# Performance work log

Hardware: AMD Instinct MI355X
Metric: run time of the kernel (lower is better)

Reference implementation:

```python
import jax, jax.numpy as jnp
import numpy as np

N_NODES = 160_000
N_EDGES = 640_000
N_GRAPHS = 8_000
IN_FEATS = 74
HID = 63
MAX_DEG = 10
PRED_HID = 128
PRED_DIM = 256
BN_EPS = 1e-5
N_LAYERS = 3
PARAM_NAMES = ['W0', 'b0', 'gamma0', 'beta0', 'W1', 'b1', 'gamma1', 'beta1', 'W2', 'b2', 'gamma2', 'beta2', 'W_ng', 'b_ng', 'W_tr', 'b_tr']


def setup_inputs() -> dict:
    key = jax.random.key(0)
    ks = jax.random.split(key, 20)
    inp = {}
    inp['feats'] = jax.random.normal(ks[0], (N_NODES, IN_FEATS), dtype=jnp.float32)
    inp['src'] = jax.random.randint(ks[1], (N_EDGES,), 0, N_NODES, dtype=jnp.int32)
    inp['dst'] = jax.random.randint(ks[2], (N_EDGES,), 0, N_NODES, dtype=jnp.int32)
    # sorted graph membership: 20 nodes per graph (batched molecular graphs)
    inp['graph_ids'] = jnp.repeat(jnp.arange(N_GRAPHS, dtype=jnp.int32), N_NODES // N_GRAPHS)
    dims = [IN_FEATS, HID, HID, HID]
    for l in range(N_LAYERS):
        fi, fo = dims[l], dims[l + 1]
        inp[f'W{l}'] = jax.random.normal(ks[3 + l], (MAX_DEG, fi, fo), dtype=jnp.float32) / np.float32(np.sqrt(fi))
        inp[f'b{l}'] = jnp.zeros((MAX_DEG, fo), dtype=jnp.float32)
        inp[f'gamma{l}'] = jnp.ones((fo,), dtype=jnp.float32)
        inp[f'beta{l}'] = jnp.zeros((fo,), dtype=jnp.float32)
    inp['W_ng'] = jax.random.normal(ks[10], (HID, PRED_HID), dtype=jnp.float32) / np.float32(np.sqrt(HID))
    inp['b_ng'] = jnp.zeros((PRED_HID,), dtype=jnp.float32)
    inp['W_tr'] = jax.random.normal(ks[11], (2 * PRED_HID, PRED_DIM), dtype=jnp.float32) / np.float32(np.sqrt(2 * PRED_HID))
    inp['b_tr'] = jnp.zeros((PRED_DIM,), dtype=jnp.float32)
    return inp


def _nf_layer(h, src, dst, deg_idx, W, b, gamma, beta):
    # message passing: sum of neighbor features via copy_u / fn.sum
    neigh = jax.ops.segment_sum(h[src], dst, num_segments=N_NODES)
    tot = h + neigh  # self + neighbor sum (Duvenaud neural fingerprint)
    # degree-bucketed linear: compute all MAX_DEG transforms, select per node by degree
    z_all = jnp.einsum('ni,kio->nko', tot, W) + b  # [N, MAX_DEG, out]
    z = jnp.take_along_axis(z_all, deg_idx[:, None, None], axis=1)[:, 0, :]  # [N, out]
    z = jax.nn.relu(z)
    # batchnorm over nodes (training-mode batch statistics, eps=1e-5)
    mu = jnp.mean(z, axis=0)
    var = jnp.var(z, axis=0)
    return (z - mu) * jax.lax.rsqrt(var + BN_EPS) * gamma + beta


def _forward(feats, src, dst, graph_ids, params):
    # in-degree per node, clamped to [1, MAX_DEG] -> weight bucket index
    deg = jax.ops.segment_sum(jnp.ones((N_EDGES,), jnp.float32), dst, num_segments=N_NODES)
    deg_idx = jnp.clip(deg.astype(jnp.int32), 1, MAX_DEG) - 1
    h = feats
    for l in range(N_LAYERS):
        h = _nf_layer(h, src, dst, deg_idx, params[f'W{l}'], params[f'b{l}'],
                      params[f'gamma{l}'], params[f'beta{l}'])
    # node_to_graph linear
    h = h @ params['W_ng'] + params['b_ng']  # [N, PRED_HID]
    # SumAndMax readout over each graph
    g_sum = jax.ops.segment_sum(h, graph_ids, num_segments=N_GRAPHS)
    g_max = jax.ops.segment_max(h, graph_ids, num_segments=N_GRAPHS)
    g = jnp.tanh(jnp.concatenate([g_sum, g_max], axis=-1))  # [G, 2*PRED_HID]
    return g @ params['W_tr'] + params['b_tr']  # [G, PRED_DIM]


def reference(feats, src, dst, graph_ids, W0, b0, gamma0, beta0, W1, b1, gamma1, beta1, W2, b2, gamma2, beta2, W_ng, b_ng, W_tr, b_tr):
    params = dict(zip(PARAM_NAMES, (W0, b0, gamma0, beta0, W1, b1, gamma1, beta1, W2, b2, gamma2, beta2, W_ng, b_ng, W_tr, b_tr)))
    return _forward(feats, src, dst, graph_ids, params)
```

## Files before the change

### kernel.cpp

```cpp
#include <hip/hip_runtime.h>
#include <stdint.h>
#include <math.h>

static constexpr int NN = 160000;
static constexpr int NE = 640000;
static constexpr int NG = 8000;
static constexpr int FH  = 63;
static constexpr int ZST = 64;
static constexpr int FST = 80;
static constexpr int NB  = 128;
static constexpr int LGRID = 1536;

static constexpr size_t OFF_DEGCNT = 0;
static constexpr size_t OFF_CURSOR = 640000;
static constexpr size_t OFF_BCNT   = 1280000;
static constexpr size_t OFF_SPART  = 1280064;
static constexpr size_t ZERO_BYTES = 1673280;
static constexpr size_t OFF_ROWPTR = 1673280;
static constexpr size_t OFF_BLKSUM = 2313472;
static constexpr size_t OFF_COL    = 2315520;
static constexpr size_t OFF_BLIST  = 4875520;
static constexpr size_t OFF_AFC    = 17675520;
static constexpr size_t OFF_WNG2   = 17677056;
static constexpr size_t OFF_BNG2   = 17709312;
static constexpr size_t OFF_PBLK   = 17709824;
static constexpr size_t OFF_FB     = 17710080;
static constexpr size_t OFF_Z0     = 43310080;
static constexpr size_t OFF_Z1     = 63790080;

__device__ __forceinline__ float blo(unsigned u) {
    union { unsigned i; float f; } v; v.i = u << 16; return v.f;
}
__device__ __forceinline__ float bhi(unsigned u) {
    union { unsigned i; float f; } v; v.i = u & 0xffff0000u; return v.f;
}
__device__ __forceinline__ unsigned short f2b(float f) {
    union { float f; unsigned i; } v; v.f = f;
    unsigned r = v.i + 0x7fffu + ((v.i >> 16) & 1u);
    return (unsigned short)(r >> 16);
}
__device__ __forceinline__ void acc8(float* a, uint4 q) {
    a[0] += blo(q.x); a[1] += bhi(q.x);
    a[2] += blo(q.y); a[3] += bhi(q.y);
    a[4] += blo(q.z); a[5] += bhi(q.z);
    a[6] += blo(q.w); a[7] += bhi(q.w);
}

__global__ void k_degree(const int* __restrict__ dst, int* __restrict__ degcnt) {
    int e = blockIdx.x * 256 + threadIdx.x;
    if (e < NE) atomicAdd(&degcnt[dst[e]], 1);
}

__global__ void k_scan1(const int* __restrict__ degcnt, int* __restrict__ row_ptr,
                        int* __restrict__ blksum) {
    __shared__ int s[1024];
    int t = threadIdx.x;
    int i = blockIdx.x * 1024 + t;
    int v = (i < NN) ? degcnt[i] : 0;
    s[t] = v; __syncthreads();
    for (int off = 1; off < 1024; off <<= 1) {
        int x = (t >= off) ? s[t - off] : 0;
        __syncthreads();
        s[t] += x;
        __syncthreads();
    }
    if (i < NN) row_ptr[i + 1] = s[t];
    if (t == 1023) blksum[blockIdx.x] = s[t];
}

__global__ void k_scan2(int* __restrict__ blksum, int nblk) {
    __shared__ int s[256];
    int t = threadIdx.x;
    int v = (t < nblk) ? blksum[t] : 0;
    s[t] = v; __syncthreads();
    for (int off = 1; off < 256; off <<= 1) {
        int x = (t >= off) ? s[t - off] : 0;
        __syncthreads();
        s[t] += x;
        __syncthreads();
    }
    if (t < nblk) blksum[t] = s[t] - v;
}

__global__ void k_scan3(int* __restrict__ row_ptr, const int* __restrict__ blksum) {
    int t = threadIdx.x;
    int i = blockIdx.x * 1024 + t;
    if (i < NN) row_ptr[i + 1] += blksum[blockIdx.x];
    if (i == 0) row_ptr[0] = 0;
}

__global__ void k_cast(const float* __restrict__ feats, unsigned short* __restrict__ fb) {
    int i = blockIdx.x * 256 + threadIdx.x;
    if (i >= NN * FST) return;
    int n = i / FST, c = i - n * FST;
    float v = (c < 74) ? feats[n * 74 + c] : 0.f;
    union { float f; unsigned u; } x; x.f = v;
    unsigned r = x.u + 0x7fffu + ((x.u >> 16) & 1u);
    fb[i] = (unsigned short)(r >> 16);
}

__global__ void __launch_bounds__(1024) k_bucket(
        const int* __restrict__ degcnt, const int* __restrict__ row_ptr,
        int* __restrict__ bcnt, int2* __restrict__ blist) {
    __shared__ int scnt[10], sbase[10];
    int tid = threadIdx.x;
    if (tid < 10) scnt[tid] = 0;
    __syncthreads();
    int n = blockIdx.x * 1024 + tid;
    int k = 0, pos = 0;
    bool v = (n < NN);
    int rp = 0;
    if (v) {
        int d = degcnt[n];
        rp = row_ptr[n];
        k = (d < 1) ? 0 : ((d > 10) ? 9 : d - 1);
        pos = atomicAdd(&scnt[k], 1);
    }
    __syncthreads();
    if (tid < 10) sbase[tid] = scnt[tid] ? atomicAdd(&bcnt[tid], scnt[tid]) : 0;
    __syncthreads();
    if (v) blist[k * NN + sbase[k] + pos] = make_int2(n, rp);
}

__global__ void k_prep(const int* __restrict__ bcnt, int* __restrict__ pblk) {
    if (threadIdx.x == 0) {
        int s = 0; pblk[0] = 0;
        for (int k = 0; k < 10; ++k) { s += (bcnt[k] + NB - 1) / NB; pblk[k + 1] = s; }
    }
}

__global__ void k_fill(const int* __restrict__ src, const int* __restrict__ dst,
                       const int* __restrict__ row_ptr, int* __restrict__ cursor,
                       int* __restrict__ col) {
    int e = blockIdx.x * 256 + threadIdx.x;
    if (e >= NE) return;
    int d = dst[e];
    int pos = row_ptr[d] + atomicAdd(&cursor[d], 1);
    col[pos] = src[e];
}

template<int FI, int IST, bool AFF>
__global__ void __launch_bounds__(256, 2) k_layer(
    const unsigned short* __restrict__ in,
    const float* __restrict__ aff,
    const int* __restrict__ row_ptr, const int* __restrict__ col,
    const int* __restrict__ bcnt, const int2* __restrict__ blist,
    const int* __restrict__ pblk,
    const float* __restrict__ W, const float* __restrict__ B,
    unsigned short* __restrict__ zout, float* __restrict__ spart)
{
    constexpr int CH = IST / 8;
    __shared__ float sW[FI * 63 + 64];
    __shared__ float sTot[4][80][8];
    __shared__ int   sN[4][8];
    __shared__ float sRed[2][4][64];

    int b = blockIdx.x;
    if (b >= pblk[10]) return;
    int k = 0;
#pragma unroll
    for (int i = 1; i <= 9; ++i) k += (b >= pblk[i]) ? 1 : 0;
    int base = (b - pblk[k]) * NB;
    int cnt = bcnt[k];
    if (base >= cnt) return;

    int tid = threadIdx.x;
    int wave = tid >> 6, lane = tid & 63;
    int t = lane >> 3, r = lane & 7;

    const float* Wk = W + (size_t)k * FI * 63;
#pragma unroll 4
    for (int i = tid; i < FI * 63; i += 256) sW[i] = Wk[i];
    __syncthreads();

    const uint4* inq = (const uint4*)in;
    float bterm = (lane < 63) ? B[k * 63 + lane] : 0.f;
    float lsum = 0.f, lsq = 0.f;

#pragma unroll 1
    for (int it = 0; it < NB / 32; ++it) {
        int idx = base + it * 32 + wave * 8 + t;
        if (base + it * 32 >= cnt) break;
        bool val = (idx < cnt);
        int2 bl = blist[k * NN + (val ? idx : (cnt - 1))];
        int n = bl.x, rs = bl.y;
        int dg = (k >= 1 && k <= 8) ? (k + 1) : (row_ptr[n + 1] - rs);
        if (r == 0) sN[wave][t] = val ? n : -1;

        float a[8] = {0.f, 0.f, 0.f, 0.f, 0.f, 0.f, 0.f, 0.f};
        {
            uint4 q = inq[(size_t)n * CH + r];
            acc8(a, q);
        }
        int d = 0;
#pragma unroll 1
        for (; d + 4 <= dg; d += 4) {
            int c0 = col[rs + d], c1 = col[rs + d + 1];
            int c2 = col[rs + d + 2], c3 = col[rs + d + 3];
            uint4 q0 = inq[(size_t)c0 * CH + r];
            uint4 q1 = inq[(size_t)c1 * CH + r];
            uint4 q2 = inq[(size_t)c2 * CH + r];
            uint4 q3 = inq[(size_t)c3 * CH + r];
            acc8(a, q0); acc8(a, q1); acc8(a, q2); acc8(a, q3);
        }
#pragma unroll 1
        for (; d < dg; ++d) {
            int c = col[rs + d];
            uint4 q = inq[(size_t)c * CH + r];
            acc8(a, q);
        }

        if constexpr (IST == 80) {
            float e2[8] = {0.f, 0.f, 0.f, 0.f, 0.f, 0.f, 0.f, 0.f};
            if (r < 2) {
                uint4 q = inq[(size_t)n * CH + 8 + r];
                acc8(e2, q);
                int d2 = 0;
#pragma unroll 1
                for (; d2 < dg; ++d2) {
                    int c = col[rs + d2];
                    uint4 p = inq[(size_t)c * CH + 8 + r];
                    acc8(e2, p);
                }
#pragma unroll
                for (int j = 0; j < 8; ++j) sTot[wave][64 + 8 * r + j][t] = e2[j];
            }
        }

        if constexpr (AFF) {
            const float4* af = (const float4*)aff;
            float4 A0 = af[2 * r], A1 = af[2 * r + 1];
            float4 C0 = af[16 + 2 * r], C1 = af[16 + 2 * r + 1];
            float dp1 = (float)(dg + 1);
            a[0] = A0.x * a[0] + dp1 * C0.x;  a[1] = A0.y * a[1] + dp1 * C0.y;
            a[2] = A0.z * a[2] + dp1 * C0.z;  a[3] = A0.w * a[3] + dp1 * C0.w;
            a[4] = A1.x * a[4] + dp1 * C1.x;  a[5] = A1.y * a[5] + dp1 * C1.y;
            a[6] = A1.z * a[6] + dp1 * C1.z;  a[7] = A1.w * a[7] + dp1 * C1.w;
        }

#pragma unroll
        for (int j = 0; j < 8; ++j) sTot[wave][8 * r + j][t] = a[j];

        float acc[8];
#pragma unroll
        for (int i = 0; i < 8; ++i) acc[i] = bterm;
#pragma unroll 4
        for (int j = 0; j < FI; ++j) {
            float w = sW[j * 63 + lane];
            float4 u = *(const float4*)&sTot[wave][j][0];
            float4 v = *(const float4*)&sTot[wave][j][4];
            acc[0] = fmaf(u.x, w, acc[0]); acc[1] = fmaf(u.y, w, acc[1]);
            acc[2] = fmaf(u.z, w, acc[2]); acc[3] = fmaf(u.w, w, acc[3]);
            acc[4] = fmaf(v.x, w, acc[4]); acc[5] = fmaf(v.y, w, acc[5]);
            acc[6] = fmaf(v.z, w, acc[6]); acc[7] = fmaf(v.w, w, acc[7]);
        }

#pragma unroll
        for (int tt = 0; tt < 8; ++tt) {
            int nn = sN[wave][tt];
            float z = fmaxf(acc[tt], 0.f);
            if (nn >= 0 && lane < 63) {
                zout[(size_t)nn * ZST + lane] = f2b(z);
                lsum += z; lsq += z * z;
            }
        }
    }

    sRed[0][wave][lane] = lsum;
    sRed[1][wave][lane] = lsq;
    __syncthreads();
    if (wave == 0 && lane < 63) {
        float s = sRed[0][0][lane] + sRed[0][1][lane] + sRed[0][2][lane] + sRed[0][3][lane];
        float q = sRed[1][0][lane] + sRed[1][1][lane] + sRed[1][2][lane] + sRed[1][3][lane];
        float* sp = spart + (size_t)(blockIdx.x & 255) * 128;
        atomicAdd(&sp[lane], s);
        atomicAdd(&sp[64 + lane], q);
    }
}

__global__ void k_bn(const float* __restrict__ spart, const float* __restrict__ gamma,
                     const float* __restrict__ beta, float* __restrict__ afc) {
    int o = threadIdx.x;
    if (o >= 63) return;
    double s = 0.0, q = 0.0;
    for (int cp = 0; cp < 256; ++cp) {
        s += (double)spart[cp * 128 + o];
        q += (double)spart[cp * 128 + 64 + o];
    }
    double mu  = s / NN;
    double var = q / NN - mu * mu;
    float a = (float)((double)gamma[o] / sqrt(var + 1e-5));
    float c = (float)((double)beta[o] - mu * (double)a);
    afc[o] = a;
    afc[64 + o] = c;
}

__global__ void k_fold(const float* __restrict__ W_ng, const float* __restrict__ b_ng,
                       const float* __restrict__ afc2, float* __restrict__ Wng2,
                       float* __restrict__ bng2) {
    int o = threadIdx.x;
    float acc = b_ng[o];
    for (int j = 0; j < 63; ++j) {
        float w = W_ng[j * 128 + o];
        Wng2[j * 128 + o] = afc2[j] * w;
        acc = fmaf(afc2[64 + j], w, acc);
    }
    bng2[o] = acc;
}

__global__ void __launch_bounds__(256) k_graph(
    const unsigned short* __restrict__ Z2, const float* __restrict__ Wng2,
    const float* __restrict__ bng2, const float* __restrict__ W_tr,
    const float* __restrict__ b_tr, float* __restrict__ out)
{
    __shared__ float sWng[64 * 128];
    __shared__ unsigned short sZ[4 * 20 * 64];
    __shared__ float sT[4][256];
    int tid = threadIdx.x;
    int g0 = blockIdx.x * 4;

#pragma unroll 4
    for (int i = tid; i < 64 * 128; i += 256)
        sWng[i] = (i < 63 * 128) ? Wng2[i] : 0.f;
    {
        const uint4* zsrc = (const uint4*)(Z2 + (size_t)g0 * 20 * ZST);
        uint4* zdst = (uint4*)sZ;
#pragma unroll 3
        for (int i = tid; i < 640; i += 256) zdst[i] = zsrc[i];
    }
    if (tid < 80) sZ[tid * 64 + 63] = 0;
    __syncthreads();

    int wv = tid >> 6, lane = tid & 63;
    const unsigned short* zg = sZ + wv * 1280;

    float acc0[20], acc1[20];
    float b0v = bng2[lane], b1v = bng2[lane + 64];
#pragma unroll
    for (int i = 0; i < 20; ++i) { acc0[i] = b0v; acc1[i] = b1v; }
#pragma unroll 1
    for (int jb = 0; jb < 16; ++jb) {
        int j = jb * 4;
        float w00 = sWng[(j + 0) * 128 + lane], w01 = sWng[(j + 0) * 128 + 64 + lane];
        float w10 = sWng[(j + 1) * 128 + lane], w11 = sWng[(j + 1) * 128 + 64 + lane];
        float w20 = sWng[(j + 2) * 128 + lane], w21 = sWng[(j + 2) * 128 + 64 + lane];
        float w30 = sWng[(j + 3) * 128 + lane], w31 = sWng[(j + 3) * 128 + 64 + lane];
#pragma unroll
        for (int i = 0; i < 20; ++i) {
            uint2 zz = *(const uint2*)&zg[i * 64 + j];
            float z0 = blo(zz.x), z1 = bhi(zz.x);
            float z2 = blo(zz.y), z3 = bhi(zz.y);
            acc0[i] = fmaf(z0, w00, acc0[i]); acc1[i] = fmaf(z0, w01, acc1[i]);
            acc0[i] = fmaf(z1, w10, acc0[i]); acc1[i] = fmaf(z1, w11, acc1[i]);
            acc0[i] = fmaf(z2, w20, acc0[i]); acc1[i] = fmaf(z2, w21, acc1[i]);
            acc0[i] = fmaf(z3, w30, acc0[i]); acc1[i] = fmaf(z3, w31, acc1[i]);
        }
    }
    float s0 = 0.f, s1 = 0.f, m0 = -1e30f, m1 = -1e30f;
#pragma unroll
    for (int i = 0; i < 20; ++i) {
        s0 += acc0[i]; s1 += acc1[i];
        m0 = fmaxf(m0, acc0[i]); m1 = fmaxf(m1, acc1[i]);
    }
    sT[wv][lane]       = tanhf(s0);
    sT[wv][lane + 64]  = tanhf(s1);
    sT[wv][128 + lane] = tanhf(m0);
    sT[wv][192 + lane] = tanhf(m1);
    __syncthreads();

    int d = tid;
    float acc[4];
    float bt = b_tr[d];
#pragma unroll
    for (int gl = 0; gl < 4; ++gl) acc[gl] = bt;
#pragma unroll 16
    for (int q = 0; q < 256; ++q) {
        float w = W_tr[q * 256 + d];
#pragma unroll
        for (int gl = 0; gl < 4; ++gl) acc[gl] = fmaf(sT[gl][q], w, acc[gl]);
    }
#pragma unroll
    for (int gl = 0; gl < 4; ++gl) out[(size_t)(g0 + gl) * 256 + d] = acc[gl];
}

extern "C" void kernel_launch(void* const* d_in, const int* in_sizes, int n_in,
                              void* d_out, int out_size, void* d_ws, size_t ws_size,
                              hipStream_t stream) {
    const float* feats = (const float*)d_in[0];
    const int*   src   = (const int*)d_in[1];
    const int*   dst   = (const int*)d_in[2];
    const float* W0 = (const float*)d_in[4];
    const float* b0 = (const float*)d_in[5];
    const float* g0 = (const float*)d_in[6];
    const float* be0 = (const float*)d_in[7];
    const float* W1 = (const float*)d_in[8];
    const float* b1 = (const float*)d_in[9];
    const float* g1 = (const float*)d_in[10];
    const float* be1 = (const float*)d_in[11];
    const float* W2 = (const float*)d_in[12];
    const float* b2 = (const float*)d_in[13];
    const float* g2 = (const float*)d_in[14];
    const float* be2 = (const float*)d_in[15];
    const float* Wng = (const float*)d_in[16];
    const float* bng = (const float*)d_in[17];
    const float* Wtr = (const float*)d_in[18];
    const float* btr = (const float*)d_in[19];
    float* out = (float*)d_out;

    char* ws = (char*)d_ws;
    int*    degcnt  = (int*)(ws + OFF_DEGCNT);
    int*    cursor  = (int*)(ws + OFF_CURSOR);
    int*    bcnt    = (int*)(ws + OFF_BCNT);
    float*  spart   = (float*)(ws + OFF_SPART);
    int*    row_ptr = (int*)(ws + OFF_ROWPTR);
    int*    blksum  = (int*)(ws + OFF_BLKSUM);
    int*    col     = (int*)(ws + OFF_COL);
    int2*   blist   = (int2*)(ws + OFF_BLIST);
    float*  afc     = (float*)(ws + OFF_AFC);
    float*  Wng2    = (float*)(ws + OFF_WNG2);
    float*  bng2    = (float*)(ws + OFF_BNG2);
    int*    pblk    = (int*)(ws + OFF_PBLK);
    unsigned short* Fb = (unsigned short*)(ws + OFF_FB);
    unsigned short* Z0 = (unsigned short*)(ws + OFF_Z0);
    unsigned short* Z1 = (unsigned short*)(ws + OFF_Z1);
    unsigned short* Z2 = Z0;

    hipMemsetAsync(d_ws, 0, ZERO_BYTES, stream);

    k_degree<<<NE / 256, 256, 0, stream>>>(dst, degcnt);
    k_cast<<<NN * FST / 256, 256, 0, stream>>>(feats, Fb);
    k_scan1<<<157, 1024, 0, stream>>>(degcnt, row_ptr, blksum);
    k_scan2<<<1, 256, 0, stream>>>(blksum, 157);
    k_scan3<<<157, 1024, 0, stream>>>(row_ptr, blksum);
    k_bucket<<<157, 1024, 0, stream>>>(degcnt, row_ptr, bcnt, blist);
    k_prep<<<1, 64, 0, stream>>>(bcnt, pblk);
    k_fill<<<NE / 256, 256, 0, stream>>>(src, dst, row_ptr, cursor, col);

    k_layer<74, FST, false><<<LGRID, 256, 0, stream>>>(
        Fb, nullptr, row_ptr, col, bcnt, blist, pblk, W0, b0, Z0, spart);
    k_bn<<<1, 64, 0, stream>>>(spart, g0, be0, afc);
    k_layer<63, ZST, true><<<LGRID, 256, 0, stream>>>(
        Z0, afc, row_ptr, col, bcnt, blist, pblk, W1, b1, Z1, spart + 256 * 128);
    k_bn<<<1, 64, 0, stream>>>(spart + 256 * 128, g1, be1, afc + 128);
    k_layer<63, ZST, true><<<LGRID, 256, 0, stream>>>(
        Z1, afc + 128, row_ptr, col, bcnt, blist, pblk, W2, b2, Z2, spart + 2 * 256 * 128);
    k_bn<<<1, 64, 0, stream>>>(spart + 2 * 256 * 128, g2, be2, afc + 256);

    k_fold<<<1, 128, 0, stream>>>(Wng, bng, afc + 256, Wng2, bng2);
    k_graph<<<NG / 4, 256, 0, stream>>>(Z2, Wng2, bng2, Wtr, btr, out);
}
```

Baseline: 516.4 us.

## Use bf16 MFMA for node-to-graph and readout transform in graph kernel

Rewrites the final graph kernel so both the node-to-graph linear and the W_tr projection run on 16x16x32 bf16 MFMA instructions instead of scalar FMAs. A new prep kernel pre-swizzles W_ng (with the batchnorm scale folded in, split into hi/lo bf16 parts for precision) and W_tr into MFMA fragment layouts. Each block now handles 16 graphs, and the per-graph sum/max are done with lane masks and cross-lane shuffles. The bias is folded analytically (20*b for the sum). This trades the fp32 path for bf16 inputs to W_tr, which adds rounding error, and uses Z1's workspace for the packed weights.

```diff
diff --git a/kernel.cpp b/kernel.cpp
--- a/kernel.cpp
+++ b/kernel.cpp
@@ -21,12 +21,13 @@
 static constexpr size_t OFF_COL    = 2315520;
 static constexpr size_t OFF_BLIST  = 4875520;
 static constexpr size_t OFF_AFC    = 17675520;
-static constexpr size_t OFF_WNG2   = 17677056;
 static constexpr size_t OFF_BNG2   = 17709312;
 static constexpr size_t OFF_PBLK   = 17709824;
 static constexpr size_t OFF_FB     = 17710080;
 static constexpr size_t OFF_Z0     = 43310080;
 static constexpr size_t OFF_Z1     = 63790080;
+static constexpr size_t OFF_WNGF   = OFF_Z1;
+static constexpr size_t OFF_WTRF   = OFF_Z1 + 32768;
 
 __device__ __forceinline__ float blo(unsigned u) {
     union { unsigned i; float f; } v; v.i = u << 16; return v.f;
@@ -45,6 +46,10 @@
     a[4] += blo(q.z); a[5] += bhi(q.z);
     a[6] += blo(q.w); a[7] += bhi(q.w);
 }
+
+typedef __attribute__((ext_vector_type(8))) short bf16x8;
+typedef __attribute__((ext_vector_type(4))) float f32x4;
+union U8 { uint4 u; bf16x8 b; };
 
 __global__ void k_degree(const int* __restrict__ dst, int* __restrict__ degcnt) {
     int e = blockIdx.x * 256 + threadIdx.x;
@@ -295,92 +300,169 @@
     afc[64 + o] = c;
 }
 
-__global__ void k_fold(const float* __restrict__ W_ng, const float* __restrict__ b_ng,
-                       const float* __restrict__ afc2, float* __restrict__ Wng2,
-                       float* __restrict__ bng2) {
-    int o = threadIdx.x;
-    float acc = b_ng[o];
-    for (int j = 0; j < 63; ++j) {
-        float w = W_ng[j * 128 + o];
-        Wng2[j * 128 + o] = afc2[j] * w;
-        acc = fmaf(afc2[64 + j], w, acc);
-    }
-    bng2[o] = acc;
-}
-
-__global__ void __launch_bounds__(256) k_graph(
-    const unsigned short* __restrict__ Z2, const float* __restrict__ Wng2,
-    const float* __restrict__ bng2, const float* __restrict__ W_tr,
+__global__ void k_prepw(const float* __restrict__ W_ng, const float* __restrict__ b_ng,
+                        const float* __restrict__ afc2, const float* __restrict__ W_tr,
+                        unsigned short* __restrict__ WngF, unsigned short* __restrict__ WtrF,
+                        float* __restrict__ bng2) {
+    int bid = blockIdx.x, tid = threadIdx.x;
+    if (bid == 0) {
+        if (tid < 128) {
+            float acc = b_ng[tid];
+            for (int j = 0; j < 63; ++j)
+                acc = fmaf(afc2[64 + j], W_ng[j * 128 + tid], acc);
+            bng2[tid] = acc;
+        }
+    } else if (bid <= 64) {
+        int idx = (bid - 1) * 256 + tid;
+        int j = idx & 7, lane = (idx >> 3) & 63;
+        int nt = (idx >> 9) & 7, kb = idx >> 12;
+        int k = (kb & 1) * 32 + ((lane >> 4) << 3) + j;
+        int col = nt * 16 + (lane & 15);
+        float w = (k < 63) ? afc2[k] * W_ng[k * 128 + col] : 0.f;
+        unsigned short hi = f2b(w);
+        if (kb < 2) WngF[idx] = hi;
+        else        WngF[idx] = f2b(w - blo(hi));
+    } else {
+        int idx = (bid - 65) * 256 + tid;
+        int j = idx & 7, lane = (idx >> 3) & 63;
+        int kb = (idx >> 9) & 7, nt = idx >> 12;
+        int k = kb * 32 + ((lane >> 4) << 3) + j;
+        int col = nt * 16 + (lane & 15);
+        WtrF[idx] = f2b(W_tr[k * 256 + col]);
+    }
+}
+
+__global__ void __launch_bounds__(256, 2) k_graph(
+    const unsigned short* __restrict__ Z2, const unsigned short* __restrict__ WngF,
+    const float* __restrict__ bng2, const unsigned short* __restrict__ WtrF,
     const float* __restrict__ b_tr, float* __restrict__ out)
 {
-    __shared__ float sWng[64 * 128];
-    __shared__ unsigned short sZ[4 * 20 * 64];
-    __shared__ float sT[4][256];
+    __shared__ unsigned short sW[16384];
+    __shared__ float sT[16 * 256];
+    __shared__ float sB[128];
+
     int tid = threadIdx.x;
-    int g0 = blockIdx.x * 4;
-
-#pragma unroll 4
-    for (int i = tid; i < 64 * 128; i += 256)
-        sWng[i] = (i < 63 * 128) ? Wng2[i] : 0.f;
+    int wave = tid >> 6, lane = tid & 63;
+    int gl15 = lane & 15, grp = lane >> 4;
+
     {
-        const uint4* zsrc = (const uint4*)(Z2 + (size_t)g0 * 20 * ZST);
-        uint4* zdst = (uint4*)sZ;
-#pragma unroll 3
-        for (int i = tid; i < 640; i += 256) zdst[i] = zsrc[i];
-    }
-    if (tid < 80) sZ[tid * 64 + 63] = 0;
-    __syncthreads();
-
-    int wv = tid >> 6, lane = tid & 63;
-    const unsigned short* zg = sZ + wv * 1280;
-
-    float acc0[20], acc1[20];
-    float b0v = bng2[lane], b1v = bng2[lane + 64];
-#pragma unroll
-    for (int i = 0; i < 20; ++i) { acc0[i] = b0v; acc1[i] = b1v; }
+        const uint4* srcq = (const uint4*)WngF;
+        uint4* dstq = (uint4*)sW;
+#pragma unroll
+        for (int i = 0; i < 8; ++i) dstq[tid + 256 * i] = srcq[tid + 256 * i];
+    }
+    if (tid < 128) sB[tid] = bng2[tid];
+    __syncthreads();
+
+    int nodeBase = blockIdx.x * 320 + wave * 80;
+    const uint4* zq = (const uint4*)Z2;
+    uint4 a0[5], a1[5];
+#pragma unroll
+    for (int m = 0; m < 5; ++m) {
+        size_t row = (size_t)(nodeBase + m * 16 + gl15) * 8;
+        a0[m] = zq[row + grp];
+        a1[m] = zq[row + 4 + grp];
+    }
+    if (grp == 3) {
+#pragma unroll
+        for (int m = 0; m < 5; ++m) a1[m].w &= 0xffffu;
+    }
+
+    const uint4* swq = (const uint4*)sW;
+    const float NEGI = -3.0e38f;
+
 #pragma unroll 1
-    for (int jb = 0; jb < 16; ++jb) {
-        int j = jb * 4;
-        float w00 = sWng[(j + 0) * 128 + lane], w01 = sWng[(j + 0) * 128 + 64 + lane];
-        float w10 = sWng[(j + 1) * 128 + lane], w11 = sWng[(j + 1) * 128 + 64 + lane];
-        float w20 = sWng[(j + 2) * 128 + lane], w21 = sWng[(j + 2) * 128 + 64 + lane];
-        float w30 = sWng[(j + 3) * 128 + lane], w31 = sWng[(j + 3) * 128 + 64 + lane];
-#pragma unroll
-        for (int i = 0; i < 20; ++i) {
-            uint2 zz = *(const uint2*)&zg[i * 64 + j];
-            float z0 = blo(zz.x), z1 = bhi(zz.x);
-            float z2 = blo(zz.y), z3 = bhi(zz.y);
-            acc0[i] = fmaf(z0, w00, acc0[i]); acc1[i] = fmaf(z0, w01, acc1[i]);
-            acc0[i] = fmaf(z1, w10, acc0[i]); acc1[i] = fmaf(z1, w11, acc1[i]);
-            acc0[i] = fmaf(z2, w20, acc0[i]); acc1[i] = fmaf(z2, w21, acc1[i]);
-            acc0[i] = fmaf(z3, w30, acc0[i]); acc1[i] = fmaf(z3, w31, acc1[i]);
-        }
-    }
-    float s0 = 0.f, s1 = 0.f, m0 = -1e30f, m1 = -1e30f;
-#pragma unroll
-    for (int i = 0; i < 20; ++i) {
-        s0 += acc0[i]; s1 += acc1[i];
-        m0 = fmaxf(m0, acc0[i]); m1 = fmaxf(m1, acc1[i]);
-    }
-    sT[wv][lane]       = tanhf(s0);
-    sT[wv][lane + 64]  = tanhf(s1);
-    sT[wv][128 + lane] = tanhf(m0);
-    sT[wv][192 + lane] = tanhf(m1);
-    __syncthreads();
-
-    int d = tid;
-    float acc[4];
-    float bt = b_tr[d];
-#pragma unroll
-    for (int gl = 0; gl < 4; ++gl) acc[gl] = bt;
-#pragma unroll 16
-    for (int q = 0; q < 256; ++q) {
-        float w = W_tr[q * 256 + d];
-#pragma unroll
-        for (int gl = 0; gl < 4; ++gl) acc[gl] = fmaf(sT[gl][q], w, acc[gl]);
-    }
-#pragma unroll
-    for (int gl = 0; gl < 4; ++gl) out[(size_t)(g0 + gl) * 256 + d] = acc[gl];
+    for (int nt = 0; nt < 8; ++nt) {
+        U8 b0, b1, b2, b3;
+        b0.u = swq[(0 * 8 + nt) * 64 + lane];
+        b1.u = swq[(1 * 8 + nt) * 64 + lane];
+        b2.u = swq[(2 * 8 + nt) * 64 + lane];
+        b3.u = swq[(3 * 8 + nt) * 64 + lane];
+
+        f32x4 ac[5];
+#pragma unroll
+        for (int m = 0; m < 5; ++m) {
+            U8 xa0, xa1; xa0.u = a0[m]; xa1.u = a1[m];
+            f32x4 c = {0.f, 0.f, 0.f, 0.f};
+            c = __builtin_amdgcn_mfma_f32_16x16x32_bf16(xa0.b, b0.b, c, 0, 0, 0);
+            c = __builtin_amdgcn_mfma_f32_16x16x32_bf16(xa1.b, b1.b, c, 0, 0, 0);
+            c = __builtin_amdgcn_mfma_f32_16x16x32_bf16(xa0.b, b2.b, c, 0, 0, 0);
+            c = __builtin_amdgcn_mfma_f32_16x16x32_bf16(xa1.b, b3.b, c, 0, 0, 0);
+            ac[m] = c;
+        }
+
+        float s[4] = {0.f, 0.f, 0.f, 0.f};
+        float x[4] = {NEGI, NEGI, NEGI, NEGI};
+        bool cA = lane < 16, cB = lane < 32, cC = lane < 48;
+#pragma unroll
+        for (int r = 0; r < 4; ++r) {
+            float v0 = ac[0][r]; s[0] += v0; x[0] = fmaxf(x[0], v0);
+            float v4 = ac[4][r]; s[3] += v4; x[3] = fmaxf(x[3], v4);
+            float v1 = ac[1][r]; float v1a = cA ? v1 : 0.f;
+            s[0] += v1a; s[1] += v1 - v1a;
+            x[0] = fmaxf(x[0], cA ? v1 : NEGI); x[1] = fmaxf(x[1], cA ? NEGI : v1);
+            float v2 = ac[2][r]; float v2a = cB ? v2 : 0.f;
+            s[1] += v2a; s[2] += v2 - v2a;
+            x[1] = fmaxf(x[1], cB ? v2 : NEGI); x[2] = fmaxf(x[2], cB ? NEGI : v2);
+            float v3 = ac[3][r]; float v3a = cC ? v3 : 0.f;
+            s[2] += v3a; s[3] += v3 - v3a;
+            x[2] = fmaxf(x[2], cC ? v3 : NEGI); x[3] = fmaxf(x[3], cC ? NEGI : v3);
+        }
+#pragma unroll
+        for (int g = 0; g < 4; ++g) {
+            s[g] += __shfl_xor(s[g], 16);
+            s[g] += __shfl_xor(s[g], 32);
+            x[g] = fmaxf(x[g], __shfl_xor(x[g], 16));
+            x[g] = fmaxf(x[g], __shfl_xor(x[g], 32));
+        }
+        if (lane < 16) {
+            int c = nt * 16 + lane;
+            float bb = sB[c];
+#pragma unroll
+            for (int g = 0; g < 4; ++g) {
+                int row = wave * 4 + g;
+                int swz = (row & 7) << 2;
+                sT[(row * 256 + c) ^ swz]       = tanhf(s[g] + 20.f * bb);
+                sT[(row * 256 + 128 + c) ^ swz] = tanhf(x[g] + bb);
+            }
+        }
+    }
+    __syncthreads();
+
+    U8 pa[8];
+    {
+        int swz = (gl15 & 7) << 2;
+#pragma unroll
+        for (int kb = 0; kb < 8; ++kb) {
+            int k8 = kb * 32 + grp * 8;
+            float4 t0 = *(const float4*)&sT[(gl15 * 256 + k8) ^ swz];
+            float4 t1 = *(const float4*)&sT[(gl15 * 256 + k8 + 4) ^ swz];
+            unsigned u0 = (unsigned)f2b(t0.x) | ((unsigned)f2b(t0.y) << 16);
+            unsigned u1 = (unsigned)f2b(t0.z) | ((unsigned)f2b(t0.w) << 16);
+            unsigned u2 = (unsigned)f2b(t1.x) | ((unsigned)f2b(t1.y) << 16);
+            unsigned u3 = (unsigned)f2b(t1.z) | ((unsigned)f2b(t1.w) << 16);
+            pa[kb].u = make_uint4(u0, u1, u2, u3);
+        }
+    }
+    const uint4* wtq = (const uint4*)WtrF;
+    size_t gbase = (size_t)blockIdx.x * 16 * 256;
+#pragma unroll 2
+    for (int i = 0; i < 4; ++i) {
+        int nt = wave * 4 + i;
+        f32x4 c = {0.f, 0.f, 0.f, 0.f};
+#pragma unroll
+        for (int kb = 0; kb < 8; ++kb) {
+            U8 b; b.u = wtq[(nt * 8 + kb) * 64 + lane];
+            c = __builtin_amdgcn_mfma_f32_16x16x32_bf16(pa[kb].b, b.b, c, 0, 0, 0);
+        }
+        int d = nt * 16 + gl15;
+        float btv = b_tr[d];
+#pragma unroll
+        for (int r = 0; r < 4; ++r) {
+            int row = grp * 4 + r;
+            out[gbase + (size_t)row * 256 + d] = c[r] + btv;
+        }
+    }
 }
 
 extern "C" void kernel_launch(void* const* d_in, const int* in_sizes, int n_in,
@@ -417,13 +499,14 @@
     int*    col     = (int*)(ws + OFF_COL);
     int2*   blist   = (int2*)(ws + OFF_BLIST);
     float*  afc     = (float*)(ws + OFF_AFC);
-    float*  Wng2    = (float*)(ws + OFF_WNG2);
     float*  bng2    = (float*)(ws + OFF_BNG2);
     int*    pblk    = (int*)(ws + OFF_PBLK);
     unsigned short* Fb = (unsigned short*)(ws + OFF_FB);
     unsigned short* Z0 = (unsigned short*)(ws + OFF_Z0);
     unsigned short* Z1 = (unsigned short*)(ws + OFF_Z1);
     unsigned short* Z2 = Z0;
+    unsigned short* WngF = (unsigned short*)(ws + OFF_WNGF);
+    unsigned short* WtrF = (unsigned short*)(ws + OFF_WTRF);
 
     hipMemsetAsync(d_ws, 0, ZERO_BYTES, stream);
 
@@ -446,6 +529,6 @@
         Z1, afc + 128, row_ptr, col, bcnt, blist, pblk, W2, b2, Z2, spart + 2 * 256 * 128);
     k_bn<<<1, 64, 0, stream>>>(spart + 2 * 256 * 128, g2, be2, afc + 256);
 
-    k_fold<<<1, 128, 0, stream>>>(Wng, bng, afc + 256, Wng2, bng2);
-    k_graph<<<NG / 4, 256, 0, stream>>>(Z2, Wng2, bng2, Wtr, btr, out);
-}
+    k_prepw<<<321, 256, 0, stream>>>(Wng, bng, afc + 256, Wtr, WngF, WtrF, bng2);
+    k_graph<<<NG / 16, 256, 0, stream>>>(Z2, WngF, bng2, WtrF, btr, out);
+}
```

Measured after the change: 450.3 us. -12.8%, faster.
